# Kernel tuning notes

Measured on AMD Instinct MI355X. Metric: run time of the kernel, lower is better.

The kernel has to match this reference:

```python
import jax, jax.numpy as jnp
import numpy as np

D_IN = 2048
D_OUT = 2048
SEQ = 4096


def setup_inputs() -> dict:
    key = jax.random.key(0)
    kx, kq, kk, kv = jax.random.split(key, 4)
    x = jax.random.normal(kx, (SEQ, D_IN), dtype=jnp.float32)
    # torch.nn.Linear weights have shape [d_out, d_in]
    s = 1.0 / np.sqrt(D_IN)
    W_q = jax.random.uniform(kq, (D_OUT, D_IN), jnp.float32, -s, s)
    W_k = jax.random.uniform(kk, (D_OUT, D_IN), jnp.float32, -s, s)
    W_v = jax.random.uniform(kv, (D_OUT, D_IN), jnp.float32, -s, s)
    return {"x": x, "W_q": W_q, "W_k": W_k, "W_v": W_v}


def reference(x, W_q, W_k, W_v):
    # projections (torch Linear: x @ W.T)
    q = x @ W_q.T  # [S, D]
    k = x @ W_k.T
    v = x @ W_v.T
    scores = q @ k.T  # [S, S]
    scale = jnp.asarray(k.shape[-1], scores.dtype) ** 0.5
    attn = jax.nn.softmax(scores / scale, axis=-1)
    # post-softmax causal mask + row renormalization (faithful to source)
    S = scores.shape[0]
    mask = jnp.tril(jnp.ones((S, S), dtype=attn.dtype))
    masked = attn * mask
    masked = masked / masked.sum(axis=1, keepdims=True)
    return masked @ v  # [S, D]
```

## Files before the change

kernel.cpp:

```cpp
#include <hip/hip_runtime.h>
#include <hip/hip_bf16.h>
#include <math.h>


typedef __attribute__((ext_vector_type(8))) short bf16x8;
typedef __attribute__((ext_vector_type(4))) float f32x4;
typedef __attribute__((ext_vector_type(8))) unsigned short u16x8;
typedef __attribute__((ext_vector_type(4))) int iv4;

__device__ __forceinline__ unsigned short f2bf(float f) {
  unsigned int u = __float_as_uint(f);
  u += 0x7FFFu + ((u >> 16) & 1u);
  return (unsigned short)(u >> 16);
}

__device__ __forceinline__ void gload16(const unsigned short* g, unsigned short* l) {
  __builtin_amdgcn_global_load_lds(
      (const __attribute__((address_space(1))) void*)g,
      (__attribute__((address_space(3))) void*)l,
      16, 0, 0);
}

template <int OFF>
__device__ __forceinline__ bf16x8 dsr(unsigned addr) {
  iv4 r;
  asm volatile("ds_read_b128 %0, %1 offset:%2" : "=v"(r) : "v"(addr), "i"(OFF));
  return __builtin_bit_cast(bf16x8, r);
}

__global__ void cvt_all(const float* __restrict__ x, const float* __restrict__ wq,
                        const float* __restrict__ wk, const float* __restrict__ wv,
                        unsigned short* __restrict__ xb, unsigned short* __restrict__ wqb,
                        unsigned short* __restrict__ wkb, unsigned short* __restrict__ wvb) {
  const int SD = 4096 * 2048, DD = 2048 * 2048;
  int i = (blockIdx.x * 256 + threadIdx.x) * 8;
  const float* in;
  unsigned short* out;
  int off;
  if (i < SD)               { in = x;  out = xb;  off = i; }
  else if (i < SD + DD)     { in = wq; out = wqb; off = i - SD; }
  else if (i < SD + 2 * DD) { in = wk; out = wkb; off = i - SD - DD; }
  else                      { in = wv; out = wvb; off = i - SD - 2 * DD; }
  float4 a = *(const float4*)(in + off);
  float4 b = *(const float4*)(in + off + 4);
  u16x8 r;
  r[0] = f2bf(a.x); r[1] = f2bf(a.y); r[2] = f2bf(a.z); r[3] = f2bf(a.w);
  r[4] = f2bf(b.x); r[5] = f2bf(b.y); r[6] = f2bf(b.z); r[7] = f2bf(b.w);
  *(u16x8*)(out + off) = r;
}

#define LGKM_SB()                                         \
  asm volatile("s_waitcnt lgkmcnt(0)" ::: "memory");      \
  __builtin_amdgcn_sched_barrier(0)

#define QMFMA(MB, NB, AF, BV)                                                 \
  _Pragma("unroll")                                                           \
  for (int _fm = 0; _fm < 4; ++_fm)                                           \
    _Pragma("unroll")                                                         \
    for (int _fn = 0; _fn < 2; ++_fn)                                         \
      _Pragma("unroll")                                                       \
      for (int _ks = 0; _ks < 2; ++_ks)                                       \
        acc[(MB) + _fm][(NB) + _fn] = __builtin_amdgcn_mfma_f32_16x16x32_bf16( \
            AF[_fm * 2 + _ks], BV[_fn * 2 + _ks], acc[(MB) + _fm][(NB) + _fn], \
            0, 0, 0);

#define STG_A(mhv, tau, bufv)                                                 \
  do {                                                                        \
    unsigned short* _d = lds + (bufv) * 32768 + (mhv) * 8192 + w * 512;       \
    gload16(pA + (size_t)((mhv) * 64) * KC + ((size_t)(tau) << 6), _d);       \
    gload16(pA + (size_t)(128 + (mhv) * 64) * KC + ((size_t)(tau) << 6),      \
            _d + 4096);                                                       \
  } while (0)

#define STG_B(nhv, tau, bufv)                                                 \
  do {                                                                        \
    unsigned short* _d = lds + (bufv) * 32768 + 16384 + (nhv) * 8192 + w * 512;\
    gload16(pB + (size_t)((nhv) * 32) * KC + ((size_t)(tau) << 6), _d);       \
    gload16(pB + (size_t)(128 + (nhv) * 32) * KC + ((size_t)(tau) << 6),      \
            _d + 4096);                                                       \
  } while (0)

#define VM_WAIT()                                                             \
  do {                                                                        \
    if (tail) { asm volatile("s_waitcnt vmcnt(0)" ::: "memory"); }            \
    else      { asm volatile("s_waitcnt vmcnt(8)" ::: "memory"); }            \
  } while (0)

template <int KC>
__device__ __forceinline__ void gemm_core(const unsigned short* __restrict__ Ab,
                                          const unsigned short* __restrict__ Bb,
                                          unsigned short* lds, int ktiles,
                                          f32x4 (&acc)[8][4]) {
  const int tid  = threadIdx.x;
  const int lane = tid & 63;
  const int w    = tid >> 6;
  const int wm   = w >> 2;
  const int wn   = w & 3;

  const int base  = w * 8 + (lane >> 3);
  const int gslot = (lane & 7) ^ ((lane >> 3) & 7);
  const unsigned short* pA = Ab + (size_t)base * KC + gslot * 8;
  const unsigned short* pB =
      Bb + (size_t)((base >> 5) * 64 + (base & 31)) * KC + gslot * 8;

  const unsigned lb = (unsigned)(size_t)&lds[0];
  const int rl = lane & 15, g = lane >> 4;
  const unsigned sw0 = (unsigned)(((0 + g) ^ (rl & 7)) * 16);
  const unsigned sw1 = (unsigned)(((4 + g) ^ (rl & 7)) * 16);
  const unsigned rA = lb + (unsigned)(wm * 8192 + rl * 128);
  const unsigned rB = lb + (unsigned)(wn * 4096 + rl * 128);

#pragma unroll
  for (int m = 0; m < 8; ++m)
#pragma unroll
    for (int n = 0; n < 4; ++n) acc[m][n] = f32x4{0.f, 0.f, 0.f, 0.f};

  STG_A(0, 0, 0); STG_B(0, 0, 0); STG_A(1, 0, 0); STG_B(1, 0, 0);
  if (ktiles > 1) {
    STG_A(0, 1, 1); STG_B(0, 1, 1); STG_A(1, 1, 1);
    asm volatile("s_waitcnt vmcnt(6)" ::: "memory");
  } else {
    asm volatile("s_waitcnt vmcnt(0)" ::: "memory");
  }
  __builtin_amdgcn_s_barrier();

  bf16x8 af0[8], af1[8], bv0[4], bv1[4];
  {
    const unsigned aA0 = rA + sw0, aA1 = rA + sw1;
    const unsigned aB0 = rB + sw0, aB1 = rB + sw1;
    af0[0] = dsr<0>(aA0);     af0[1] = dsr<0>(aA1);
    af0[2] = dsr<2048>(aA0);  af0[3] = dsr<2048>(aA1);
    af0[4] = dsr<4096>(aA0);  af0[5] = dsr<4096>(aA1);
    af0[6] = dsr<6144>(aA0);  af0[7] = dsr<6144>(aA1);
    bv0[0] = dsr<32768>(aB0); bv0[1] = dsr<32768>(aB1);
    bv0[2] = dsr<34816>(aB0); bv0[3] = dsr<34816>(aB1);
  }

  for (int t = 0; t < ktiles; ++t) {
    const unsigned bo  = (unsigned)(t & 1) << 16;
    const unsigned bon = (unsigned)((t + 1) & 1) << 16;
    const int buf = t & 1, nb = (t + 1) & 1;
    const bool s1 = (t + 1) < ktiles, s2 = (t + 2) < ktiles;
    const bool tail = t >= ktiles - 2;
    const unsigned aA0 = rA + bo + sw0, aA1 = rA + bo + sw1;
    const unsigned aB0 = rB + bo + sw0, aB1 = rB + bo + sw1;
    const unsigned nA0 = rA + bon + sw0, nA1 = rA + bon + sw1;
    const unsigned nB0 = rB + bon + sw0, nB1 = rB + bon + sw1;

    LGKM_SB();
    __builtin_amdgcn_s_setprio(1);
    QMFMA(0, 0, af0, bv0);
    __builtin_amdgcn_s_setprio(0);
    af1[0] = dsr<16384>(aA0); af1[1] = dsr<16384>(aA1);
    af1[2] = dsr<18432>(aA0); af1[3] = dsr<18432>(aA1);
    af1[4] = dsr<20480>(aA0); af1[5] = dsr<20480>(aA1);
    af1[6] = dsr<22528>(aA0); af1[7] = dsr<22528>(aA1);
    if (s1) STG_B(1, t + 1, nb);
    VM_WAIT();
    __builtin_amdgcn_s_barrier();

    LGKM_SB();
    __builtin_amdgcn_s_setprio(1);
    QMFMA(4, 0, af1, bv0);
    __builtin_amdgcn_s_setprio(0);
    bv1[0] = dsr<49152>(aB0); bv1[1] = dsr<49152>(aB1);
    bv1[2] = dsr<51200>(aB0); bv1[3] = dsr<51200>(aB1);
    if (s2) { STG_A(0, t + 2, buf); STG_B(0, t + 2, buf); }
    VM_WAIT();
    __builtin_amdgcn_s_barrier();

    LGKM_SB();
    __builtin_amdgcn_s_setprio(1);
    QMFMA(0, 2, af0, bv1);
    __builtin_amdgcn_s_setprio(0);
    if (s1) {
      af0[0] = dsr<0>(nA0);     af0[1] = dsr<0>(nA1);
      af0[2] = dsr<2048>(nA0);  af0[3] = dsr<2048>(nA1);
      af0[4] = dsr<4096>(nA0);  af0[5] = dsr<4096>(nA1);
      af0[6] = dsr<6144>(nA0);  af0[7] = dsr<6144>(nA1);
      bv0[0] = dsr<32768>(nB0); bv0[1] = dsr<32768>(nB1);
      bv0[2] = dsr<34816>(nB0); bv0[3] = dsr<34816>(nB1);
    }
    if (s2) STG_A(1, t + 2, buf);
    VM_WAIT();
    __builtin_amdgcn_s_barrier();

    __builtin_amdgcn_sched_barrier(0);
    __builtin_amdgcn_s_setprio(1);
    QMFMA(4, 2, af1, bv1);
    __builtin_amdgcn_s_setprio(0);
    VM_WAIT();
    __builtin_amdgcn_s_barrier();
  }
}

__device__ __forceinline__ void ep_f32(float* C, const f32x4 (&acc)[8][4],
                                       int r0, int c0, int ldc, float scale) {
  const int lane = threadIdx.x & 63, w = threadIdx.x >> 6;
  const int crow0 = r0 + (w >> 2) * 128 + ((lane >> 4) << 2);
  const int ccol0 = c0 + (w & 3) * 64 + (lane & 15);
#pragma unroll
  for (int m = 0; m < 8; ++m)
#pragma unroll
    for (int n = 0; n < 4; ++n)
#pragma unroll
      for (int j = 0; j < 4; ++j)
        C[(size_t)(crow0 + m * 16 + j) * ldc + (ccol0 + n * 16)] =
            acc[m][n][j] * scale;
}

__device__ __forceinline__ void ep_f32_at(float* C, const f32x4 (&acc)[8][4],
                                          int r0, int c0, int ldc, float scale) {
  const int lane = threadIdx.x & 63, w = threadIdx.x >> 6;
  const int crow0 = r0 + (w >> 2) * 128 + ((lane >> 4) << 2);
  const int ccol0 = c0 + (w & 3) * 64 + (lane & 15);
#pragma unroll
  for (int m = 0; m < 8; ++m)
#pragma unroll
    for (int n = 0; n < 4; ++n)
#pragma unroll
      for (int j = 0; j < 4; ++j)
        atomicAdd(&C[(size_t)(crow0 + m * 16 + j) * ldc + (ccol0 + n * 16)],
                  acc[m][n][j] * scale);
}

__device__ __forceinline__ void ep_bf16(unsigned short* C, const f32x4 (&acc)[8][4],
                                        int r0, int c0, int ldc) {
  const int lane = threadIdx.x & 63, w = threadIdx.x >> 6;
  const int crow0 = r0 + (w >> 2) * 128 + ((lane >> 4) << 2);
  const int ccol0 = c0 + (w & 3) * 64 + (lane & 15);
#pragma unroll
  for (int m = 0; m < 8; ++m)
#pragma unroll
    for (int n = 0; n < 4; ++n)
#pragma unroll
      for (int j = 0; j < 4; ++j)
        C[(size_t)(crow0 + m * 16 + j) * ldc + (ccol0 + n * 16)] =
            f2bf(acc[m][n][j]);
}

__global__ __launch_bounds__(512, 2)
void proj_qk(const unsigned short* __restrict__ xb,
             const unsigned short* __restrict__ wqb,
             const unsigned short* __restrict__ wkb,
             unsigned short* __restrict__ Q, unsigned short* __restrict__ Kb) {
  __shared__ __align__(16) unsigned short lds[65536];
  const int bid = blockIdx.x;
  const int wg = (bid & 7) * 32 + (bid >> 3);
  const int bm = wg >> 4, bnr = wg & 15;
  const unsigned short* B = (bnr < 8) ? wqb : wkb;
  unsigned short* C = (bnr < 8) ? Q : Kb;
  const int bnl = bnr & 7;
  f32x4 acc[8][4];
  gemm_core<2048>(xb + (size_t)bm * 256 * 2048, B + (size_t)bnl * 256 * 2048,
                  lds, 32, acc);
  ep_bf16(C, acc, bm * 256, bnl * 256, 2048);
}

__global__ __launch_bounds__(512, 2)
void vt_qkt(const unsigned short* __restrict__ Qp,
            const unsigned short* __restrict__ Kp,
            const unsigned short* __restrict__ wvb,
            const unsigned short* __restrict__ xb,
            float* __restrict__ sc, unsigned short* __restrict__ Vt,
            float scale) {
  __shared__ __align__(16) unsigned short lds[65536];
  const int id = blockIdx.x;
  f32x4 acc[8][4];
  if (id < 64) {
    const int p = id >> 2, c = id & 3;
    const size_t koff = (size_t)c * 8 * 64;
    gemm_core<2048>(Qp + (size_t)15 * 256 * 2048 + koff,
                    Kp + (size_t)p * 256 * 2048 + koff, lds, 8, acc);
    ep_f32_at(sc, acc, 3840, p * 256, 4096, scale);
  } else if (id < 184) {
    const int q = id - 64;
    int bm = 0;
    while ((bm + 1) * (bm + 2) / 2 <= q) ++bm;
    const int bn = q - bm * (bm + 1) / 2;
    gemm_core<2048>(Qp + (size_t)bm * 256 * 2048,
                    Kp + (size_t)bn * 256 * 2048, lds, 32, acc);
    ep_f32(sc, acc, bm * 256, bn * 256, 4096, scale);
  } else {
    const int v = id - 184, bm = v >> 4, bn = v & 15;
    gemm_core<2048>(wvb + (size_t)bm * 256 * 2048,
                    xb + (size_t)bn * 256 * 2048, lds, 32, acc);
    ep_bf16(Vt, acc, bm * 256, bn * 256, 4096);
  }
}

__global__ __launch_bounds__(512, 2)
void pv_q(const unsigned short* __restrict__ P,
          const unsigned short* __restrict__ Vt, float* __restrict__ out,
          float* __restrict__ aux1, float* __restrict__ aux2,
          float* __restrict__ aux3, int* __restrict__ ctr) {
  __shared__ __align__(16) unsigned short lds[65536];
  __shared__ int sid;
  f32x4 acc[8][4];
  for (;;) {
    if (threadIdx.x == 0) sid = atomicAdd(ctr, 1);
    __syncthreads();
    const int id = sid;
    if (id >= 320) return;
    int rem = id, bm = 15, s = 4;
    for (;;) {
      s = (bm >> 2) + 1;
      const int cnt = 8 * s;
      if (rem < cnt) break;
      rem -= cnt;
      --bm;
    }
    const int bn = rem / s, p = rem % s;
    const int kt = (bm + 1) * 4;
    const int k0 = (kt * p) / s, k1 = (kt * (p + 1)) / s;
    gemm_core<4096>(P + (size_t)bm * 256 * 4096 + (size_t)k0 * 64,
                    Vt + (size_t)bn * 256 * 4096 + (size_t)k0 * 64,
                    lds, k1 - k0, acc);
    if (p == 0)      ep_f32(out,  acc, bm * 256,        bn * 256, 2048, 1.0f);
    else if (p == 1) ep_f32(aux1, acc, bm * 256 - 1024, bn * 256, 2048, 1.0f);
    else if (p == 2) ep_f32(aux2, acc, bm * 256 - 2048, bn * 256, 2048, 1.0f);
    else             ep_f32(aux3, acc, bm * 256 - 3072, bn * 256, 2048, 1.0f);
  }
}

__global__ void add3(float* __restrict__ out, const float* __restrict__ aux1,
                     const float* __restrict__ aux2, const float* __restrict__ aux3) {
  const size_t i = ((size_t)blockIdx.x * 256 + threadIdx.x) * 8;
  const int row = 1024 + (int)(i >> 11);
  float* o = out + (size_t)1024 * 2048 + i;
  f32x4 a0 = *(const f32x4*)o;
  f32x4 a1 = *(const f32x4*)(o + 4);
  a0 += *(const f32x4*)(aux1 + i);
  a1 += *(const f32x4*)(aux1 + i + 4);
  if (row >= 2048) {
    const size_t j = i - (size_t)1024 * 2048;
    a0 += *(const f32x4*)(aux2 + j);
    a1 += *(const f32x4*)(aux2 + j + 4);
  }
  if (row >= 3072) {
    const size_t j = i - (size_t)2048 * 2048;
    a0 += *(const f32x4*)(aux3 + j);
    a1 += *(const f32x4*)(aux3 + j + 4);
  }
  *(f32x4*)o = a0;
  *(f32x4*)(o + 4) = a1;
}

__global__ void softmax_causal(const float* __restrict__ Sc,
                               unsigned short* __restrict__ P, int S) {
  const int i = blockIdx.x;
  const int tid = threadIdx.x;
  const int nvalid = i + 1;
  const int pad_end = ((i >> 8) + 1) << 8;
  const float* row = Sc + (size_t)i * S;

  float v[16];
  float m = -1e30f;
#pragma unroll
  for (int it = 0; it < 16; ++it) {
    const int j = tid + it * 256;
    const float x = (j < nvalid) ? row[j] : -1e30f;
    v[it] = x;
    m = fmaxf(m, x);
  }
#pragma unroll
  for (int d = 1; d < 64; d <<= 1) m = fmaxf(m, __shfl_xor(m, d));
  __shared__ float red_m[4], red_s[4];
  const int lane = tid & 63, wv = tid >> 6;
  if (lane == 0) red_m[wv] = m;
  __syncthreads();
  m = fmaxf(fmaxf(red_m[0], red_m[1]), fmaxf(red_m[2], red_m[3]));

  float s = 0.0f;
#pragma unroll
  for (int it = 0; it < 16; ++it) {
    const int j = tid + it * 256;
    const float e = (j < nvalid) ? __expf(v[it] - m) : 0.0f;
    v[it] = e;
    s += e;
  }
#pragma unroll
  for (int d = 1; d < 64; d <<= 1) s += __shfl_xor(s, d);
  if (lane == 0) red_s[wv] = s;
  __syncthreads();
  s = red_s[0] + red_s[1] + red_s[2] + red_s[3];

  const float inv = 1.0f / s;
  unsigned short* prow = P + (size_t)i * S;
#pragma unroll
  for (int it = 0; it < 16; ++it) {
    const int j = tid + it * 256;
    if (j < pad_end) prow[j] = (j < nvalid) ? f2bf(v[it] * inv) : (unsigned short)0;
  }
}

extern "C" void kernel_launch(void* const* d_in, const int* in_sizes, int n_in,
                              void* d_out, int out_size, void* d_ws, size_t ws_size,
                              hipStream_t stream) {
  const float* x  = (const float*)d_in[0];
  const float* Wq = (const float*)d_in[1];
  const float* Wk = (const float*)d_in[2];
  const float* Wv = (const float*)d_in[3];
  float* out = (float*)d_out;

  const int S = 4096, D = 2048;
  char* ws = (char*)d_ws;
  const size_t MB = 1u << 20;
  float*          sc   = (float*)ws;
  float*          aux1 = (float*)ws;
  float*          aux2 = (float*)(ws + 24 * MB);
  float*          aux3 = (float*)(ws + 40 * MB);
  unsigned short* xb   = (unsigned short*)(ws + 64 * MB);
  unsigned short* wqb  = (unsigned short*)(ws + 80 * MB);
  unsigned short* wkb  = (unsigned short*)(ws + 88 * MB);
  unsigned short* wvb  = (unsigned short*)(ws + 96 * MB);
  unsigned short* Q    = (unsigned short*)(ws + 104 * MB);
  unsigned short* Kb   = (unsigned short*)(ws + 120 * MB);
  unsigned short* Vt   = (unsigned short*)(ws + 80 * MB);
  unsigned short* P    = (unsigned short*)(ws + 104 * MB);
  int*            ctr  = (int*)(ws + 136 * MB);

  cvt_all<<<(S * D + 3 * D * D) / (256 * 8), 256, 0, stream>>>(
      x, Wq, Wk, Wv, xb, wqb, wkb, wvb);

  hipMemsetAsync(ctr, 0, 16, stream);
  hipMemsetAsync(sc + (size_t)3840 * 4096, 0, (size_t)256 * 4096 * 4, stream);

  proj_qk<<<256, 512, 0, stream>>>(xb, wqb, wkb, Q, Kb);

  const float scale = 1.0f / sqrtf((float)D);
  vt_qkt<<<312, 512, 0, stream>>>(Q, Kb, wvb, xb, sc, Vt, scale);

  softmax_causal<<<S, 256, 0, stream>>>(sc, P, S);

  pv_q<<<256, 512, 0, stream>>>(P, Vt, out, aux1, aux2, aux3, ctr);
  add3<<<3072, 256, 0, stream>>>(out, aux1, aux2, aux3);
}
```

Before: 238.9 us.

## Restructure GEMM K-loop to two barriers and store split-K partials in bf16

The GEMM main loop goes from four barrier phases per k-tile to two. All LDS fragment reads for the tile are issued up front, and the global-to-LDS stage loads are moved after the MFMA blocks with adjusted vmcnt waits. Separately, the split-K partial sums in the PV kernel are written as bf16 instead of fp32, and add3 widens them back. This halves the traffic for the partial buffers, at the cost of an extra rounding step on the partial sums and a changed load-wait schedule that could expose latency or hazards.

New measurement: 237.6 us. No clear change (-0.5%).

```diff
diff --git a/kernel.cpp b/kernel.cpp
--- a/kernel.cpp
+++ b/kernel.cpp
@@ -12,6 +12,9 @@
   unsigned int u = __float_as_uint(f);
   u += 0x7FFFu + ((u >> 16) & 1u);
   return (unsigned short)(u >> 16);
+}
+__device__ __forceinline__ float bf2f(unsigned short u) {
+  return __uint_as_float((unsigned int)u << 16);
 }
 
 __device__ __forceinline__ void gload16(const unsigned short* g, unsigned short* l) {
@@ -80,12 +83,6 @@
             _d + 4096);                                                       \
   } while (0)
 
-#define VM_WAIT()                                                             \
-  do {                                                                        \
-    if (tail) { asm volatile("s_waitcnt vmcnt(0)" ::: "memory"); }            \
-    else      { asm volatile("s_waitcnt vmcnt(8)" ::: "memory"); }            \
-  } while (0)
-
 template <int KC>
 __device__ __forceinline__ void gemm_core(const unsigned short* __restrict__ Ab,
                                           const unsigned short* __restrict__ Bb,
@@ -148,28 +145,27 @@
     const unsigned nB0 = rB + bon + sw0, nB1 = rB + bon + sw1;
 
     LGKM_SB();
-    __builtin_amdgcn_s_setprio(1);
-    QMFMA(0, 0, af0, bv0);
-    __builtin_amdgcn_s_setprio(0);
     af1[0] = dsr<16384>(aA0); af1[1] = dsr<16384>(aA1);
     af1[2] = dsr<18432>(aA0); af1[3] = dsr<18432>(aA1);
     af1[4] = dsr<20480>(aA0); af1[5] = dsr<20480>(aA1);
     af1[6] = dsr<22528>(aA0); af1[7] = dsr<22528>(aA1);
-    if (s1) STG_B(1, t + 1, nb);
-    VM_WAIT();
-    __builtin_amdgcn_s_barrier();
-
+    bv1[0] = dsr<49152>(aB0); bv1[1] = dsr<49152>(aB1);
+    bv1[2] = dsr<51200>(aB0); bv1[3] = dsr<51200>(aB1);
+    __builtin_amdgcn_sched_barrier(0);
+    __builtin_amdgcn_s_setprio(1);
+    QMFMA(0, 0, af0, bv0);
+    __builtin_amdgcn_s_setprio(0);
     LGKM_SB();
     __builtin_amdgcn_s_setprio(1);
     QMFMA(4, 0, af1, bv0);
     __builtin_amdgcn_s_setprio(0);
-    bv1[0] = dsr<49152>(aB0); bv1[1] = dsr<49152>(aB1);
-    bv1[2] = dsr<51200>(aB0); bv1[3] = dsr<51200>(aB1);
+    if (s1) STG_B(1, t + 1, nb);
     if (s2) { STG_A(0, t + 2, buf); STG_B(0, t + 2, buf); }
-    VM_WAIT();
+    if (tail) { asm volatile("s_waitcnt vmcnt(0)" ::: "memory"); }
+    else      { asm volatile("s_waitcnt vmcnt(8)" ::: "memory"); }
     __builtin_amdgcn_s_barrier();
 
-    LGKM_SB();
+    __builtin_amdgcn_sched_barrier(0);
     __builtin_amdgcn_s_setprio(1);
     QMFMA(0, 2, af0, bv1);
     __builtin_amdgcn_s_setprio(0);
@@ -181,15 +177,13 @@
       bv0[0] = dsr<32768>(nB0); bv0[1] = dsr<32768>(nB1);
       bv0[2] = dsr<34816>(nB0); bv0[3] = dsr<34816>(nB1);
     }
-    if (s2) STG_A(1, t + 2, buf);
-    VM_WAIT();
-    __builtin_amdgcn_s_barrier();
-
     __builtin_amdgcn_sched_barrier(0);
     __builtin_amdgcn_s_setprio(1);
     QMFMA(4, 2, af1, bv1);
     __builtin_amdgcn_s_setprio(0);
-    VM_WAIT();
+    if (s2) STG_A(1, t + 2, buf);
+    if (tail) { asm volatile("s_waitcnt vmcnt(0)" ::: "memory"); }
+    else      { asm volatile("s_waitcnt vmcnt(6)" ::: "memory"); }
     __builtin_amdgcn_s_barrier();
   }
 }
@@ -292,8 +286,8 @@
 __global__ __launch_bounds__(512, 2)
 void pv_q(const unsigned short* __restrict__ P,
           const unsigned short* __restrict__ Vt, float* __restrict__ out,
-          float* __restrict__ aux1, float* __restrict__ aux2,
-          float* __restrict__ aux3, int* __restrict__ ctr) {
+          unsigned short* __restrict__ aux1, unsigned short* __restrict__ aux2,
+          unsigned short* __restrict__ aux3, int* __restrict__ ctr) {
   __shared__ __align__(16) unsigned short lds[65536];
   __shared__ int sid;
   f32x4 acc[8][4];
@@ -316,31 +310,35 @@
     gemm_core<4096>(P + (size_t)bm * 256 * 4096 + (size_t)k0 * 64,
                     Vt + (size_t)bn * 256 * 4096 + (size_t)k0 * 64,
                     lds, k1 - k0, acc);
-    if (p == 0)      ep_f32(out,  acc, bm * 256,        bn * 256, 2048, 1.0f);
-    else if (p == 1) ep_f32(aux1, acc, bm * 256 - 1024, bn * 256, 2048, 1.0f);
-    else if (p == 2) ep_f32(aux2, acc, bm * 256 - 2048, bn * 256, 2048, 1.0f);
-    else             ep_f32(aux3, acc, bm * 256 - 3072, bn * 256, 2048, 1.0f);
-  }
-}
-
-__global__ void add3(float* __restrict__ out, const float* __restrict__ aux1,
-                     const float* __restrict__ aux2, const float* __restrict__ aux3) {
+    if (p == 0)      ep_f32(out,   acc, bm * 256,        bn * 256, 2048, 1.0f);
+    else if (p == 1) ep_bf16(aux1, acc, bm * 256 - 1024, bn * 256, 2048);
+    else if (p == 2) ep_bf16(aux2, acc, bm * 256 - 2048, bn * 256, 2048);
+    else             ep_bf16(aux3, acc, bm * 256 - 3072, bn * 256, 2048);
+  }
+}
+
+__global__ void add3(float* __restrict__ out, const unsigned short* __restrict__ aux1,
+                     const unsigned short* __restrict__ aux2,
+                     const unsigned short* __restrict__ aux3) {
   const size_t i = ((size_t)blockIdx.x * 256 + threadIdx.x) * 8;
   const int row = 1024 + (int)(i >> 11);
   float* o = out + (size_t)1024 * 2048 + i;
   f32x4 a0 = *(const f32x4*)o;
   f32x4 a1 = *(const f32x4*)(o + 4);
-  a0 += *(const f32x4*)(aux1 + i);
-  a1 += *(const f32x4*)(aux1 + i + 4);
+  u16x8 b = *(const u16x8*)(aux1 + i);
+#pragma unroll
+  for (int k = 0; k < 4; ++k) { a0[k] += bf2f(b[k]); a1[k] += bf2f(b[k + 4]); }
   if (row >= 2048) {
     const size_t j = i - (size_t)1024 * 2048;
-    a0 += *(const f32x4*)(aux2 + j);
-    a1 += *(const f32x4*)(aux2 + j + 4);
+    u16x8 c = *(const u16x8*)(aux2 + j);
+#pragma unroll
+    for (int k = 0; k < 4; ++k) { a0[k] += bf2f(c[k]); a1[k] += bf2f(c[k + 4]); }
   }
   if (row >= 3072) {
     const size_t j = i - (size_t)2048 * 2048;
-    a0 += *(const f32x4*)(aux3 + j);
-    a1 += *(const f32x4*)(aux3 + j + 4);
+    u16x8 d = *(const u16x8*)(aux3 + j);
+#pragma unroll
+    for (int k = 0; k < 4; ++k) { a0[k] += bf2f(d[k]); a1[k] += bf2f(d[k + 4]); }
   }
   *(f32x4*)o = a0;
   *(f32x4*)(o + 4) = a1;
@@ -407,9 +405,9 @@
   char* ws = (char*)d_ws;
   const size_t MB = 1u << 20;
   float*          sc   = (float*)ws;
-  float*          aux1 = (float*)ws;
-  float*          aux2 = (float*)(ws + 24 * MB);
-  float*          aux3 = (float*)(ws + 40 * MB);
+  unsigned short* aux1 = (unsigned short*)ws;
+  unsigned short* aux2 = (unsigned short*)(ws + 16 * MB);
+  unsigned short* aux3 = (unsigned short*)(ws + 28 * MB);
   unsigned short* xb   = (unsigned short*)(ws + 64 * MB);
   unsigned short* wqb  = (unsigned short*)(ws + 80 * MB);
   unsigned short* wkb  = (unsigned short*)(ws + 88 * MB);
```
